# Performance work log

Hardware: AMD Instinct MI355X
Metric: run time of the kernel (lower is better)

Reference implementation:

```python
import jax, jax.numpy as jnp
import numpy as np

N_NODES = 100000
N_EDGES = 1000000
IN, HID, HEADS, OUT = 256, 32, 4, 40
HH = HID * HEADS  # 128
NEG_SLOPE = 0.2


def gat_conv(x, W, al, ar, b, src, dst, heads):
    """DGL-style GATConv. x:[N,Din] W:[Din,heads*F] al/ar/b:[heads,F]. Returns [N,heads,F]."""
    N = x.shape[0]
    h = (x @ W).reshape(N, heads, -1)                      # [N,H,F]
    el = (h * al).sum(-1)                                  # [N,H]
    er = (h * ar).sum(-1)                                  # [N,H]
    e = jax.nn.leaky_relu(el[src] + er[dst], NEG_SLOPE)    # [E,H]
    # segment softmax over incoming edges of each dst node
    m = jax.ops.segment_max(e, dst, num_segments=N)        # [N,H]
    m = jnp.where(jnp.isfinite(m), m, 0.0)                 # nodes w/o in-edges
    ex = jnp.exp(e - m[dst])                               # [E,H]
    s = jax.ops.segment_sum(ex, dst, num_segments=N)       # [N,H]
    alpha = ex / jnp.where(s[dst] == 0, 1.0, s[dst])       # [E,H]
    out = jax.ops.segment_sum(alpha[:, :, None] * h[src], dst, num_segments=N)
    return out + b                                          # [N,H,F]


def setup_inputs() -> dict:
    key = jax.random.key(0)
    ks = jax.random.split(key, 12)
    p = lambda k, shape, fan: jax.random.normal(k, shape, jnp.float32) / np.float32(np.sqrt(fan))
    features = jax.random.normal(ks[0], (N_NODES, IN), jnp.float32)
    src = jax.random.randint(ks[1], (N_EDGES,), 0, N_NODES, jnp.int32)
    dst = jax.random.randint(ks[2], (N_EDGES,), 0, N_NODES, jnp.int32)
    W1 = p(ks[3], (IN, HH), IN)
    al1 = p(ks[4], (HEADS, HID), HID)
    ar1 = p(ks[5], (HEADS, HID), HID)
    b1 = jnp.zeros((HEADS, HID), jnp.float32)
    W2 = p(ks[6], (HH, HH), HH)
    al2 = p(ks[7], (HEADS, HID), HID)
    ar2 = p(ks[8], (HEADS, HID), HID)
    b2 = jnp.zeros((HEADS, HID), jnp.float32)
    W3 = p(ks[9], (HH, OUT), HH)
    al3 = p(ks[10], (1, OUT), OUT)
    ar3 = p(ks[11], (1, OUT), OUT)
    b3 = jnp.zeros((1, OUT), jnp.float32)
    return dict(features=features, W1=W1, al1=al1, ar1=ar1, b1=b1,
                W2=W2, al2=al2, ar2=ar2, b2=b2,
                W3=W3, al3=al3, ar3=ar3, b3=b3, src=src, dst=dst)


def reference(features, W1, al1, ar1, b1, W2, al2, ar2, b2, W3, al3, ar3, b3, src, dst):
    N = features.shape[0]
    h = jax.nn.relu(gat_conv(features, W1, al1, ar1, b1, src, dst, HEADS).reshape(N, -1))
    h = jax.nn.relu(gat_conv(h, W2, al2, ar2, b2, src, dst, HEADS).reshape(N, -1))
    # dropout: eval mode -> identity
    h = gat_conv(h, W3, al3, ar3, b3, src, dst, 1).mean(1)  # [N,OUT]
    return jax.nn.log_softmax(h, axis=1)
```

## Files before the change

kernel.cpp:

```cpp
#include <hip/hip_runtime.h>
#include <hip/hip_bf16.h>
#include <math.h>

#define NN 100000
#define NE 1000000
#define CAP 128
#define NPB 512
#define NBUC ((NN + NPB - 1) / NPB)
#define CAPB 8192
#define P1B 512
#define P1E ((NE + P1B - 1) / P1B)

typedef __attribute__((ext_vector_type(8))) short bf16x8;
typedef __attribute__((ext_vector_type(4))) float f32x4;
typedef unsigned int u32;
typedef unsigned short u16;
typedef unsigned long long u64;

__device__ __forceinline__ u16 f2b(float f) {
    __hip_bfloat16 h = __float2bfloat16(f);
    return *reinterpret_cast<u16*>(&h);
}
__device__ __forceinline__ float b2f(u16 u) {
    __hip_bfloat16 h = *reinterpret_cast<__hip_bfloat16*>(&u);
    return __bfloat162float(h);
}
__device__ __forceinline__ float bflo(u32 v) { return __uint_as_float(v << 16); }
__device__ __forceinline__ float bfhi(u32 v) { return __uint_as_float(v & 0xffff0000u); }


__global__ void hist_kernel(const int* __restrict__ dst, int* __restrict__ deg, int E) {
    int i = blockIdx.x * blockDim.x + threadIdx.x;
    if (i < E) atomicAdd(&deg[dst[i]], 1);
}

__global__ void scan_local(const int* __restrict__ deg, int* __restrict__ rowptr,
                           int* __restrict__ bsum, int N) {
    __shared__ int s[256];
    int i = blockIdx.x * 256 + threadIdx.x;
    int v = (i < N) ? deg[i] : 0;
    s[threadIdx.x] = v;
    __syncthreads();
    #pragma unroll
    for (int off = 1; off < 256; off <<= 1) {
        int t = (threadIdx.x >= off) ? s[threadIdx.x - off] : 0;
        __syncthreads();
        s[threadIdx.x] += t;
        __syncthreads();
    }
    if (i < N) rowptr[i + 1] = s[threadIdx.x];
    if (threadIdx.x == 255) bsum[blockIdx.x] = s[255];
}

__global__ void scan_bsum(int* __restrict__ bsum, int NB) {
    __shared__ int s[512];
    int v = (threadIdx.x < NB) ? bsum[threadIdx.x] : 0;
    s[threadIdx.x] = v;
    __syncthreads();
    for (int off = 1; off < 512; off <<= 1) {
        int t = (threadIdx.x >= off) ? s[threadIdx.x - off] : 0;
        __syncthreads();
        s[threadIdx.x] += t;
        __syncthreads();
    }
    if (threadIdx.x < NB) bsum[threadIdx.x] = s[threadIdx.x] - v;
}

__global__ void scan_add(int* __restrict__ rowptr, const int* __restrict__ bsum, int N) {
    int i = blockIdx.x * blockDim.x + threadIdx.x;
    if (i < N) rowptr[i + 1] += bsum[i >> 8];
    if (i == 0) rowptr[0] = 0;
}


__global__ void initcur(const int* __restrict__ rowptr, int* __restrict__ gcur) {
    int b = threadIdx.x;
    if (b < NBUC) gcur[b] = rowptr[b << 9];
}

__global__ __launch_bounds__(256) void part1(const int* __restrict__ src,
                                             const int* __restrict__ dst,
                                             int* __restrict__ gcur,
                                             long long* __restrict__ ebuf) {
    __shared__ int cnt[256], sex[256], base[256], cur2[256], scn[256];
    __shared__ long long stage[P1E];
    const int tid = threadIdx.x;
    const int e0 = blockIdx.x * P1E;
    const int e1 = min(e0 + P1E, NE);
    cnt[tid] = 0;
    __syncthreads();
    for (int i = e0 + tid; i < e1; i += 256)
        atomicAdd(&cnt[dst[i] >> 9], 1);
    __syncthreads();
    int v = cnt[tid];
    scn[tid] = v;
    __syncthreads();
    #pragma unroll
    for (int off = 1; off < 256; off <<= 1) {
        int t = (tid >= off) ? scn[tid - off] : 0;
        __syncthreads();
        scn[tid] += t;
        __syncthreads();
    }
    sex[tid] = scn[tid] - v;
    if (tid < NBUC) base[tid] = (v > 0) ? atomicAdd(&gcur[tid], v) : 0;
    cur2[tid] = 0;
    __syncthreads();
    for (int i = e0 + tid; i < e1; i += 256) {
        int d = dst[i], s = src[i];
        int b = d >> 9;
        int slot = sex[b] + atomicAdd(&cur2[b], 1);
        stage[slot] = ((long long)(u32)d << 32) | (u32)s;
    }
    __syncthreads();
    const int tot = e1 - e0;
    for (int i = tid; i < tot; i += 256) {
        long long ll = stage[i];
        int b = (int)((u64)ll >> 32) >> 9;
        ebuf[(size_t)base[b] + (i - sex[b])] = ll;
    }
}

__global__ __launch_bounds__(256) void part2(const int* __restrict__ rowptr,
                                             const long long* __restrict__ ebuf,
                                             int* __restrict__ csrc) {
    __shared__ int nb[NPB], cnt[NPB];
    __shared__ int stage[CAPB];
    const int tid = threadIdx.x;
    const int n0 = blockIdx.x << 9;
    const int nn = min(NPB, NN - n0);
    const int estart = rowptr[n0];
    const int eend = rowptr[n0 + nn];
    const int tot = eend - estart;
    for (int i = tid; i < nn; i += 256) {
        nb[i] = rowptr[n0 + i] - estart;
        cnt[i] = 0;
    }
    __syncthreads();
    if (tot <= CAPB) {
        for (int i = estart + tid; i < eend; i += 256) {
            long long ll = ebuf[i];
            int ln = (int)((u64)ll >> 32) - n0;
            int pos = nb[ln] + atomicAdd(&cnt[ln], 1);
            stage[pos] = (int)ll;
        }
        __syncthreads();
        for (int i = tid; i < tot; i += 256) csrc[estart + i] = stage[i];
    } else {
        for (int i = estart + tid; i < eend; i += 256) {
            long long ll = ebuf[i];
            int ln = (int)((u64)ll >> 32) - n0;
            int pos = nb[ln] + atomicAdd(&cnt[ln], 1);
            csrc[estart + pos] = (int)ll;
        }
    }
}


__global__ void transW3(const float* __restrict__ W1, u16* __restrict__ W1t,
                        const float* __restrict__ W2, u16* __restrict__ W2t,
                        const float* __restrict__ W3, u16* __restrict__ W3t) {
    int idx = blockIdx.x * 256 + threadIdx.x;
    if (idx < 32768) {
        int n = idx / 256, k = idx % 256;
        W1t[idx] = f2b(W1[(size_t)k * 128 + n]);
    } else if (idx < 32768 + 16384) {
        int j = idx - 32768;
        int n = j / 128, k = j % 128;
        W2t[j] = f2b(W2[(size_t)k * 128 + n]);
    } else if (idx < 32768 + 16384 + 6144) {
        int j = idx - 32768 - 16384;
        int n = j / 128, k = j % 128;
        W3t[j] = f2b((n < 40) ? W3[(size_t)k * 40 + n] : 0.f);
    }
}

template<int K, int NT, int OUTW, bool AF32, int NH>
__global__ __launch_bounds__(256, 4) void gemm_s(const void* __restrict__ Ap_,
                                                 const u16* __restrict__ Wt,
                                                 const float* __restrict__ al,
                                                 const float* __restrict__ ar,
                                                 u16* __restrict__ C,
                                                 float* __restrict__ el,
                                                 float* __restrict__ er, int M) {
    constexpr int KC = 128;
    constexpr int NKC = K / KC;
    constexpr int NB = NT * 16;
    constexpr int CHK = KC / 8;
    __shared__ u16 lB[NB * KC];
    const int tid = threadIdx.x;
    const int w = tid >> 6, l = tid & 63;
    const int lr = l & 15, lq = l >> 4;
    const int row0 = blockIdx.x * 64 + w * 16;
    const u16* Ab = (const u16*)Ap_;
    const float* Af = (const float*)Ap_;

    int gr0 = row0 + lr; if (gr0 >= M) gr0 = M - 1;
    const size_t aoff = (size_t)gr0 * K;

    f32x4 acc[NT] = {};
    #pragma unroll
    for (int kc = 0; kc < NKC; ++kc) {
        for (int idx = tid; idx < NB * CHK; idx += 256) {
            int row = idx / CHK, c = idx % CHK;
            float4 v = *reinterpret_cast<const float4*>(&Wt[(size_t)row * K + kc * KC + c * 8]);
            int cs = c ^ (row & 7);
            *reinterpret_cast<float4*>(&lB[row * KC + cs * 8]) = v;
        }
        __syncthreads();
        bf16x8 a0, a1, a2, a3;
        if (AF32) {
            float4 v[8];
            #pragma unroll
            for (int i = 0; i < 8; ++i)
                v[i] = *reinterpret_cast<const float4*>(
                    &Af[aoff + kc * KC + (i >> 1) * 32 + lq * 8 + (i & 1) * 4]);
            bf16x8 t[4];
            #pragma unroll
            for (int i = 0; i < 4; ++i) {
                t[i][0] = (short)f2b(v[2 * i].x); t[i][1] = (short)f2b(v[2 * i].y);
                t[i][2] = (short)f2b(v[2 * i].z); t[i][3] = (short)f2b(v[2 * i].w);
                t[i][4] = (short)f2b(v[2 * i + 1].x); t[i][5] = (short)f2b(v[2 * i + 1].y);
                t[i][6] = (short)f2b(v[2 * i + 1].z); t[i][7] = (short)f2b(v[2 * i + 1].w);
            }
            a0 = t[0]; a1 = t[1]; a2 = t[2]; a3 = t[3];
        } else {
            a0 = *reinterpret_cast<const bf16x8*>(&Ab[aoff + kc * KC + 0 * 32 + lq * 8]);
            a1 = *reinterpret_cast<const bf16x8*>(&Ab[aoff + kc * KC + 1 * 32 + lq * 8]);
            a2 = *reinterpret_cast<const bf16x8*>(&Ab[aoff + kc * KC + 2 * 32 + lq * 8]);
            a3 = *reinterpret_cast<const bf16x8*>(&Ab[aoff + kc * KC + 3 * 32 + lq * 8]);
        }
        #pragma unroll
        for (int ks = 0; ks < 4; ++ks) {
            bf16x8 aF = (ks == 0) ? a0 : (ks == 1) ? a1 : (ks == 2) ? a2 : a3;
            const int cs = (ks * 4 + lq) ^ (lr & 7);
            #pragma unroll
            for (int nr = 0; nr < NT; ++nr) {
                bf16x8 bF = *reinterpret_cast<const bf16x8*>(&lB[(nr * 16 + lr) * KC + cs * 8]);
                acc[nr] = __builtin_amdgcn_mfma_f32_16x16x32_bf16(aF, bF, acc[nr], 0, 0, 0);
            }
        }
        if (kc + 1 < NKC) __syncthreads();
    }

    float alv[NT], arv[NT];
    #pragma unroll
    for (int nr = 0; nr < NT; ++nr) {
        int c = nr * 16 + lr;
        alv[nr] = (c < OUTW) ? al[c] : 0.f;
        arv[nr] = (c < OUTW) ? ar[c] : 0.f;
    }
    #pragma unroll
    for (int reg = 0; reg < 4; ++reg) {
        int gr = row0 + lq * 4 + reg;
        bool ok = gr < M;
        if (ok) {
            #pragma unroll
            for (int nr = 0; nr < NT; ++nr) {
                int gc = nr * 16 + lr;
                if (gc < OUTW) C[(size_t)gr * OUTW + gc] = f2b(acc[nr][reg]);
            }
        }
        float pl[NH] = {}, pr[NH] = {};
        #pragma unroll
        for (int nr = 0; nr < NT; ++nr) {
            int hidx = (NH == 1) ? 0 : (nr >> 1);
            pl[hidx] = fmaf(acc[nr][reg], alv[nr], pl[hidx]);
            pr[hidx] = fmaf(acc[nr][reg], arv[nr], pr[hidx]);
        }
        #pragma unroll
        for (int o = 8; o >= 1; o >>= 1) {
            #pragma unroll
            for (int hh = 0; hh < NH; ++hh) {
                pl[hh] += __shfl_xor(pl[hh], o);
                pr[hh] += __shfl_xor(pr[hh], o);
            }
        }
        if (ok && lr == 0) {
            #pragma unroll
            for (int hh = 0; hh < NH; ++hh) {
                el[gr * NH + hh] = pl[hh];
                er[gr * NH + hh] = pr[hh];
            }
        }
    }
}


template<bool RELU>
__global__ __launch_bounds__(256) void agg4v5(const char* __restrict__ hbase,
                                              const float4* __restrict__ el4,
                                              const float4* __restrict__ er4,
                                              const float* __restrict__ bias,
                                              const int* __restrict__ rowptr,
                                              const int* __restrict__ csrc,
                                              u32* __restrict__ out, int N) {
    __shared__ u32 s_ed[4][CAP][8];
    const int wslot = threadIdx.x >> 6, lane = threadIdx.x & 63;
    const int wid = blockIdx.x * 4 + wslot;
    if (wid >= N) return;
    const int beg = rowptr[wid];
    const int deg = rowptr[wid + 1] - beg;
    const float4 er = er4[wid];
    const int hh = lane >> 4;
    const u32 lshl = (u32)(lane << 2);
    const float2 bv = reinterpret_cast<const float2*>(bias)[lane];
    float accA, accB, invs;

    if (deg <= CAP) {
        for (int basej = 0; basej < deg; basej += 64) {
            int j = basej + lane;
            if (j < deg) {
                int sid = csrc[beg + j];
                float4 ev = el4[sid];
                float e0 = ev.x + er.x; e0 = e0 > 0.f ? e0 : 0.2f * e0;
                float e1 = ev.y + er.y; e1 = e1 > 0.f ? e1 : 0.2f * e1;
                float e2 = ev.z + er.z; e2 = e2 > 0.f ? e2 : 0.2f * e2;
                float e3 = ev.w + er.w; e3 = e3 > 0.f ? e3 : 0.2f * e3;
                u32 so = (u32)sid << 8;
                int2 v0 = make_int2(__float_as_int(__expf(e0)), (int)so);
                int2 v1 = make_int2(__float_as_int(__expf(e1)), (int)so);
                int2 v2 = make_int2(__float_as_int(__expf(e2)), (int)so);
                int2 v3 = make_int2(__float_as_int(__expf(e3)), (int)so);
                *reinterpret_cast<int2*>(&s_ed[wslot][j][0]) = v0;
                *reinterpret_cast<int2*>(&s_ed[wslot][j][2]) = v1;
                *reinterpret_cast<int2*>(&s_ed[wslot][j][4]) = v2;
                *reinterpret_cast<int2*>(&s_ed[wslot][j][6]) = v3;
            }
        }
        const u32* ebase = &s_ed[wslot][0][hh * 2];
        float a[8] = {}, b[8] = {}, sw[8] = {};
        int p = 0;
        const int deg8 = deg & ~7;
        for (; p < deg8; p += 8) {
            #pragma unroll
            for (int k = 0; k < 8; ++k) {
                int2 rv = *reinterpret_cast<const int2*>(ebase + (p + k) * 8);
                float wg = __int_as_float(rv.x);
                u32 hv = *reinterpret_cast<const u32*>(hbase + ((u32)rv.y | lshl));
                a[k] = fmaf(wg, bflo(hv), a[k]);
                b[k] = fmaf(wg, bfhi(hv), b[k]);
                sw[k] += wg;
            }
        }
        for (; p < deg; ++p) {
            int2 rv = *reinterpret_cast<const int2*>(ebase + p * 8);
            float wg = __int_as_float(rv.x);
            u32 hv = *reinterpret_cast<const u32*>(hbase + ((u32)rv.y | lshl));
            a[0] = fmaf(wg, bflo(hv), a[0]);
            b[0] = fmaf(wg, bfhi(hv), b[0]);
            sw[0] += wg;
        }
        accA = ((a[0] + a[1]) + (a[2] + a[3])) + ((a[4] + a[5]) + (a[6] + a[7]));
        accB = ((b[0] + b[1]) + (b[2] + b[3])) + ((b[4] + b[5]) + (b[6] + b[7]));
        float s = ((sw[0] + sw[1]) + (sw[2] + sw[3])) + ((sw[4] + sw[5]) + (sw[6] + sw[7]));
        invs = (deg > 0) ? 1.f / s : 0.f;
    } else {
        float er_h = hh == 0 ? er.x : hh == 1 ? er.y : hh == 2 ? er.z : er.w;
        float s = 0.f;
        accA = 0.f; accB = 0.f;
        for (int q = beg; q < beg + deg; ++q) {
            int sid = csrc[q];
            float4 ev = el4[sid];
            float e = (hh == 0 ? ev.x : hh == 1 ? ev.y : hh == 2 ? ev.z : ev.w) + er_h;
            e = e > 0.f ? e : 0.2f * e;
            float pe = __expf(e);
            u32 hv = *reinterpret_cast<const u32*>(hbase + (((u32)sid << 8) | lshl));
            s += pe;
            accA = fmaf(pe, bflo(hv), accA);
            accB = fmaf(pe, bfhi(hv), accB);
        }
        invs = 1.f / s;
    }
    float oA = accA * invs + bv.x;
    float oB = accB * invs + bv.y;
    if (RELU) { oA = fmaxf(oA, 0.f); oB = fmaxf(oB, 0.f); }
    out[(size_t)wid * 64 + lane] = ((u32)f2b(oB) << 16) | (u32)f2b(oA);
}

__global__ __launch_bounds__(256) void agg1v5(const char* __restrict__ hbase,
                                              const float* __restrict__ el,
                                              const float* __restrict__ er,
                                              const float* __restrict__ bias,
                                              const int* __restrict__ rowptr,
                                              const int* __restrict__ csrc,
                                              float* __restrict__ out, int N) {
    __shared__ u32 s_ed[4][CAP][2];
    const int wslot = threadIdx.x >> 6, lane = threadIdx.x & 63;
    const int wid = blockIdx.x * 4 + wslot;
    if (wid >= N) return;
    const int beg = rowptr[wid];
    const int deg = rowptr[wid + 1] - beg;
    const float ern = er[wid];
    const int ll = lane < 40 ? lane : 39;
    const u32 lloff = (u32)(ll << 1);
    float acc, invs;

    if (deg <= CAP) {
        for (int basej = 0; basej < deg; basej += 64) {
            int j = basej + lane;
            if (j < deg) {
                int sid = csrc[beg + j];
                float e = el[sid] + ern; e = e > 0.f ? e : 0.2f * e;
                u32 so = (u32)sid * 80u;
                *reinterpret_cast<int2*>(&s_ed[wslot][j][0]) =
                    make_int2(__float_as_int(__expf(e)), (int)so);
            }
        }
        const u32* ebase = &s_ed[wslot][0][0];
        float a[8] = {}, sw[8] = {};
        int p = 0;
        const int deg8 = deg & ~7;
        for (; p < deg8; p += 8) {
            #pragma unroll
            for (int k = 0; k < 8; ++k) {
                int2 rv = *reinterpret_cast<const int2*>(ebase + (p + k) * 2);
                float wg = __int_as_float(rv.x);
                u16 hv = *reinterpret_cast<const u16*>(hbase + ((u32)rv.y + lloff));
                a[k] = fmaf(wg, b2f(hv), a[k]);
                sw[k] += wg;
            }
        }
        for (; p < deg; ++p) {
            int2 rv = *reinterpret_cast<const int2*>(ebase + p * 2);
            float wg = __int_as_float(rv.x);
            u16 hv = *reinterpret_cast<const u16*>(hbase + ((u32)rv.y + lloff));
            a[0] = fmaf(wg, b2f(hv), a[0]);
            sw[0] += wg;
        }
        acc = ((a[0] + a[1]) + (a[2] + a[3])) + ((a[4] + a[5]) + (a[6] + a[7]));
        float s = ((sw[0] + sw[1]) + (sw[2] + sw[3])) + ((sw[4] + sw[5]) + (sw[6] + sw[7]));
        invs = (deg > 0) ? 1.f / s : 0.f;
    } else {
        float s = 0.f;
        acc = 0.f;
        for (int q = beg; q < beg + deg; ++q) {
            int sid = csrc[q];
            float e = el[sid] + ern; e = e > 0.f ? e : 0.2f * e;
            float pe = __expf(e);
            u16 hv = *reinterpret_cast<const u16*>(hbase + ((u32)sid * 80u + lloff));
            s += pe;
            acc = fmaf(pe, b2f(hv), acc);
        }
        invs = 1.f / s;
    }
    float v = acc * invs + ((lane < 40) ? bias[lane] : 0.f);
    float vv = (lane < 40) ? v : -INFINITY;
    float mx = vv;
    #pragma unroll
    for (int o = 32; o >= 1; o >>= 1) mx = fmaxf(mx, __shfl_xor(mx, o));
    float ex = (lane < 40) ? __expf(v - mx) : 0.f;
    float se = ex;
    #pragma unroll
    for (int o = 32; o >= 1; o >>= 1) se += __shfl_xor(se, o);
    if (lane < 40) out[(size_t)wid * 40 + lane] = v - mx - logf(se);
}


extern "C" void kernel_launch(void* const* d_in, const int* in_sizes, int n_in,
                              void* d_out, int out_size, void* d_ws, size_t ws_size,
                              hipStream_t stream) {
    const float* feat = (const float*)d_in[0];
    const float* W1  = (const float*)d_in[1];
    const float* al1 = (const float*)d_in[2];
    const float* ar1 = (const float*)d_in[3];
    const float* b1  = (const float*)d_in[4];
    const float* W2  = (const float*)d_in[5];
    const float* al2 = (const float*)d_in[6];
    const float* ar2 = (const float*)d_in[7];
    const float* b2  = (const float*)d_in[8];
    const float* W3  = (const float*)d_in[9];
    const float* al3 = (const float*)d_in[10];
    const float* ar3 = (const float*)d_in[11];
    const float* b3  = (const float*)d_in[12];
    const int*   src = (const int*)d_in[13];
    const int*   dst = (const int*)d_in[14];
    float* out = (float*)d_out;
    const int N = NN, E = NE;

    char* ws = (char*)d_ws;
    size_t off = 0;
    auto alloc = [&](size_t bytes) -> char* {
        char* p = ws + off;
        off += (bytes + 255) & ~(size_t)255;
        return p;
    };
    int* deg    = (int*)alloc((size_t)N * 4);
    int* rowptr = (int*)alloc((size_t)(N + 1) * 4);
    int* bsum   = (int*)alloc(512 * 4);
    int* gcur   = (int*)alloc(256 * 4);
    int* csrc   = (int*)alloc((size_t)E * 4);
    long long* ebuf = (long long*)alloc((size_t)E * 8);
    float* el   = (float*)alloc((size_t)N * 4 * 4);
    float* er   = (float*)alloc((size_t)N * 4 * 4);
    u16* hb     = (u16*)alloc((size_t)N * 128 * 2);
    u16* xb     = (u16*)alloc((size_t)N * 128 * 2);
    u16* h3     = (u16*)alloc((size_t)N * 40 * 2 + 256);
    u16* W1t    = (u16*)alloc((size_t)128 * 256 * 2);
    u16* W2t    = (u16*)alloc((size_t)128 * 128 * 2);
    u16* W3t    = (u16*)alloc((size_t)48 * 128 * 2);

    hipMemsetAsync(deg, 0, (size_t)N * 4, stream);
    hist_kernel<<<(E + 255) / 256, 256, 0, stream>>>(dst, deg, E);
    int NB = (N + 255) / 256;
    scan_local<<<NB, 256, 0, stream>>>(deg, rowptr, bsum, N);
    scan_bsum<<<1, 512, 0, stream>>>(bsum, NB);
    scan_add<<<(N + 255) / 256, 256, 0, stream>>>(rowptr, bsum, N);
    initcur<<<1, 256, 0, stream>>>(rowptr, gcur);
    part1<<<P1B, 256, 0, stream>>>(src, dst, gcur, ebuf);
    part2<<<NBUC, 256, 0, stream>>>(rowptr, ebuf, csrc);

    transW3<<<(32768 + 16384 + 6144 + 255) / 256, 256, 0, stream>>>(W1, W1t, W2, W2t, W3, W3t);

    int gemmGrid = (N + 63) / 64;
    int nodeGrid = (N + 3) / 4;

    gemm_s<256, 8, 128, true, 4><<<gemmGrid, 256, 0, stream>>>(feat, W1t, al1, ar1, hb, el, er, N);
    agg4v5<true><<<nodeGrid, 256, 0, stream>>>((const char*)hb, (const float4*)el, (const float4*)er,
                                               b1, rowptr, csrc, (u32*)xb, N);

    gemm_s<128, 8, 128, false, 4><<<gemmGrid, 256, 0, stream>>>(xb, W2t, al2, ar2, hb, el, er, N);
    agg4v5<true><<<nodeGrid, 256, 0, stream>>>((const char*)hb, (const float4*)el, (const float4*)er,
                                               b2, rowptr, csrc, (u32*)xb, N);

    gemm_s<128, 3, 40, false, 1><<<gemmGrid, 256, 0, stream>>>(xb, W3t, al3, ar3, h3, el, er, N);
    agg1v5<<<nodeGrid, 256, 0, stream>>>((const char*)h3, el, er, b3, rowptr, csrc, out, N);
}
```

Measured before the change: 330.7 us.

## Build CSR from bucket counts and aggregate two nodes per wave with block-shared edge staging

The per-node histogram and three-stage scan are replaced by a coarse 512-node bucket count and a single-block scan. Per-node row pointers are now computed inside the second partition pass with a local count and scan. The aggregation kernels handle 8 nodes per block (two per wave). Edge weights for the whole block are staged cooperatively in shared memory, and the two nodes' gathers are interleaved to increase memory-level parallelism. This cuts launch count and atomic traffic in CSR construction, at the cost of an extra ebuf read pass and more register use in the aggregation kernels.

```diff
diff --git a/kernel.cpp b/kernel.cpp
--- a/kernel.cpp
+++ b/kernel.cpp
@@ -4,12 +4,12 @@
 
 #define NN 100000
 #define NE 1000000
-#define CAP 128
 #define NPB 512
 #define NBUC ((NN + NPB - 1) / NPB)
 #define CAPB 8192
 #define P1B 512
 #define P1E ((NE + P1B - 1) / P1B)
+#define BCAP 512
 
 typedef __attribute__((ext_vector_type(8))) short bf16x8;
 typedef __attribute__((ext_vector_type(4))) float f32x4;
@@ -29,54 +29,39 @@
 __device__ __forceinline__ float bfhi(u32 v) { return __uint_as_float(v & 0xffff0000u); }
 
 
-__global__ void hist_kernel(const int* __restrict__ dst, int* __restrict__ deg, int E) {
-    int i = blockIdx.x * blockDim.x + threadIdx.x;
-    if (i < E) atomicAdd(&deg[dst[i]], 1);
-}
-
-__global__ void scan_local(const int* __restrict__ deg, int* __restrict__ rowptr,
-                           int* __restrict__ bsum, int N) {
+__global__ void bucket_cnt(const int* __restrict__ dst, int* __restrict__ bcnt, int E) {
+    __shared__ int c[NBUC];
+    for (int i = threadIdx.x; i < NBUC; i += 256) c[i] = 0;
+    __syncthreads();
+    int i = blockIdx.x * 256 + threadIdx.x;
+    const int stride = gridDim.x * 256;
+    for (; i < E; i += stride) atomicAdd(&c[dst[i] >> 9], 1);
+    __syncthreads();
+    for (int j = threadIdx.x; j < NBUC; j += 256)
+        if (c[j]) atomicAdd(&bcnt[j], c[j]);
+}
+
+__global__ void bucket_scan(const int* __restrict__ bcnt, int* __restrict__ bbase,
+                            int* __restrict__ gcur) {
     __shared__ int s[256];
-    int i = blockIdx.x * 256 + threadIdx.x;
-    int v = (i < N) ? deg[i] : 0;
-    s[threadIdx.x] = v;
-    __syncthreads();
-    #pragma unroll
+    const int tid = threadIdx.x;
+    int v = (tid < NBUC) ? bcnt[tid] : 0;
+    s[tid] = v;
+    __syncthreads();
     for (int off = 1; off < 256; off <<= 1) {
-        int t = (threadIdx.x >= off) ? s[threadIdx.x - off] : 0;
-        __syncthreads();
-        s[threadIdx.x] += t;
-        __syncthreads();
-    }
-    if (i < N) rowptr[i + 1] = s[threadIdx.x];
-    if (threadIdx.x == 255) bsum[blockIdx.x] = s[255];
-}
-
-__global__ void scan_bsum(int* __restrict__ bsum, int NB) {
-    __shared__ int s[512];
-    int v = (threadIdx.x < NB) ? bsum[threadIdx.x] : 0;
-    s[threadIdx.x] = v;
-    __syncthreads();
-    for (int off = 1; off < 512; off <<= 1) {
-        int t = (threadIdx.x >= off) ? s[threadIdx.x - off] : 0;
-        __syncthreads();
-        s[threadIdx.x] += t;
-        __syncthreads();
-    }
-    if (threadIdx.x < NB) bsum[threadIdx.x] = s[threadIdx.x] - v;
-}
-
-__global__ void scan_add(int* __restrict__ rowptr, const int* __restrict__ bsum, int N) {
-    int i = blockIdx.x * blockDim.x + threadIdx.x;
-    if (i < N) rowptr[i + 1] += bsum[i >> 8];
-    if (i == 0) rowptr[0] = 0;
-}
-
-
-__global__ void initcur(const int* __restrict__ rowptr, int* __restrict__ gcur) {
-    int b = threadIdx.x;
-    if (b < NBUC) gcur[b] = rowptr[b << 9];
-}
+        int t = (tid >= off) ? s[tid - off] : 0;
+        __syncthreads();
+        s[tid] += t;
+        __syncthreads();
+    }
+    if (tid < NBUC) {
+        int excl = s[tid] - v;
+        bbase[tid] = excl;
+        gcur[tid] = excl;
+    }
+    if (tid == NBUC - 1) bbase[NBUC] = s[tid];
+}
+
 
 __global__ __launch_bounds__(256) void part1(const int* __restrict__ src,
                                              const int* __restrict__ dst,
@@ -121,21 +106,45 @@
     }
 }
 
-__global__ __launch_bounds__(256) void part2(const int* __restrict__ rowptr,
-                                             const long long* __restrict__ ebuf,
-                                             int* __restrict__ csrc) {
+__global__ __launch_bounds__(256) void part2B(const int* __restrict__ bbase,
+                                              const long long* __restrict__ ebuf,
+                                              int* __restrict__ rowptr,
+                                              int* __restrict__ csrc) {
     __shared__ int nb[NPB], cnt[NPB];
     __shared__ int stage[CAPB];
+    __shared__ int ssum[256];
     const int tid = threadIdx.x;
     const int n0 = blockIdx.x << 9;
     const int nn = min(NPB, NN - n0);
-    const int estart = rowptr[n0];
-    const int eend = rowptr[n0 + nn];
+    const int estart = bbase[blockIdx.x];
+    const int eend = bbase[blockIdx.x + 1];
     const int tot = eend - estart;
-    for (int i = tid; i < nn; i += 256) {
-        nb[i] = rowptr[n0 + i] - estart;
-        cnt[i] = 0;
-    }
+    for (int i = tid; i < NPB; i += 256) cnt[i] = 0;
+    __syncthreads();
+    for (int i = estart + tid; i < eend; i += 256) {
+        int ln = (int)((u64)ebuf[i] >> 32) - n0;
+        atomicAdd(&cnt[ln], 1);
+    }
+    __syncthreads();
+    int a = cnt[2 * tid], b = cnt[2 * tid + 1];
+    int ts = a + b;
+    ssum[tid] = ts;
+    __syncthreads();
+    #pragma unroll
+    for (int off = 1; off < 256; off <<= 1) {
+        int t = (tid >= off) ? ssum[tid - off] : 0;
+        __syncthreads();
+        ssum[tid] += t;
+        __syncthreads();
+    }
+    int eb = ssum[tid] - ts;
+    nb[2 * tid] = eb;
+    nb[2 * tid + 1] = eb + a;
+    if (2 * tid < nn)     rowptr[n0 + 2 * tid]     = estart + eb;
+    if (2 * tid + 1 < nn) rowptr[n0 + 2 * tid + 1] = estart + eb + a;
+    if (tid == 0 && blockIdx.x == gridDim.x - 1) rowptr[NN] = eend;
+    __syncthreads();
+    for (int i = tid; i < NPB; i += 256) cnt[i] = 0;
     __syncthreads();
     if (tot <= CAPB) {
         for (int i = estart + tid; i < eend; i += 256) {
@@ -288,172 +297,256 @@
 
 
 template<bool RELU>
-__global__ __launch_bounds__(256) void agg4v5(const char* __restrict__ hbase,
+__global__ __launch_bounds__(256) void agg4v6(const char* __restrict__ hbase,
                                               const float4* __restrict__ el4,
                                               const float4* __restrict__ er4,
                                               const float* __restrict__ bias,
                                               const int* __restrict__ rowptr,
                                               const int* __restrict__ csrc,
                                               u32* __restrict__ out, int N) {
-    __shared__ u32 s_ed[4][CAP][8];
-    const int wslot = threadIdx.x >> 6, lane = threadIdx.x & 63;
-    const int wid = blockIdx.x * 4 + wslot;
-    if (wid >= N) return;
-    const int beg = rowptr[wid];
-    const int deg = rowptr[wid + 1] - beg;
-    const float4 er = er4[wid];
+    __shared__ u32 s_ed[BCAP][8];
+    __shared__ int s_off[9];
+    const int tid = threadIdx.x, w = tid >> 6, lane = tid & 63;
+    const int base = blockIdx.x * 8;
+    if (tid < 9) {
+        int n = base + tid;
+        s_off[tid] = rowptr[n <= N ? n : N];
+    }
+    __syncthreads();
+    const int beg_blk = s_off[0];
+    const int T = s_off[8] - beg_blk;
     const int hh = lane >> 4;
     const u32 lshl = (u32)(lane << 2);
     const float2 bv = reinterpret_cast<const float2*>(bias)[lane];
-    float accA, accB, invs;
-
-    if (deg <= CAP) {
-        for (int basej = 0; basej < deg; basej += 64) {
-            int j = basej + lane;
-            if (j < deg) {
-                int sid = csrc[beg + j];
+    const bool small = (T <= BCAP);
+
+    if (small) {
+        for (int t = tid; t < T; t += 256) {
+            int sid = csrc[beg_blk + t];
+            int nd = 0;
+            #pragma unroll
+            for (int k = 1; k < 8; ++k) nd += (t >= (s_off[k] - beg_blk)) ? 1 : 0;
+            float4 er = er4[base + nd];
+            float4 ev = el4[sid];
+            float e0 = ev.x + er.x; e0 = e0 > 0.f ? e0 : 0.2f * e0;
+            float e1 = ev.y + er.y; e1 = e1 > 0.f ? e1 : 0.2f * e1;
+            float e2 = ev.z + er.z; e2 = e2 > 0.f ? e2 : 0.2f * e2;
+            float e3 = ev.w + er.w; e3 = e3 > 0.f ? e3 : 0.2f * e3;
+            u32 so = (u32)sid << 8;
+            *reinterpret_cast<int2*>(&s_ed[t][0]) = make_int2(__float_as_int(__expf(e0)), (int)so);
+            *reinterpret_cast<int2*>(&s_ed[t][2]) = make_int2(__float_as_int(__expf(e1)), (int)so);
+            *reinterpret_cast<int2*>(&s_ed[t][4]) = make_int2(__float_as_int(__expf(e2)), (int)so);
+            *reinterpret_cast<int2*>(&s_ed[t][6]) = make_int2(__float_as_int(__expf(e3)), (int)so);
+        }
+    }
+    __syncthreads();
+
+    const int nA = base + 2 * w;
+    if (nA >= N) return;
+    const int nB = nA + 1;
+    float aA[4] = {}, bA[4] = {}, sA[4] = {};
+    float aB[4] = {}, bB[4] = {}, sB[4] = {};
+
+    if (small) {
+        const int oA0 = s_off[2 * w] - beg_blk, oA1 = s_off[2 * w + 1] - beg_blk;
+        const int oB0 = oA1, oB1 = s_off[2 * w + 2] - beg_blk;
+        const int dA = oA1 - oA0, dB = oB1 - oB0;
+        const int it = max((dA + 3) >> 2, (dB + 3) >> 2);
+        for (int i = 0; i < it; ++i) {
+            const int pA = oA0 + i * 4, pB = oB0 + i * 4;
+            #pragma unroll
+            for (int k = 0; k < 4; ++k) {
+                int j = pA + k; bool v = j < oA1;
+                int2 rv = *reinterpret_cast<const int2*>(&s_ed[v ? j : 0][hh * 2]);
+                float wg = v ? __int_as_float(rv.x) : 0.f;
+                u32 hv = *reinterpret_cast<const u32*>(hbase + ((u32)rv.y | lshl));
+                aA[k] = fmaf(wg, bflo(hv), aA[k]);
+                bA[k] = fmaf(wg, bfhi(hv), bA[k]);
+                sA[k] += wg;
+            }
+            #pragma unroll
+            for (int k = 0; k < 4; ++k) {
+                int j = pB + k; bool v = j < oB1;
+                int2 rv = *reinterpret_cast<const int2*>(&s_ed[v ? j : 0][hh * 2]);
+                float wg = v ? __int_as_float(rv.x) : 0.f;
+                u32 hv = *reinterpret_cast<const u32*>(hbase + ((u32)rv.y | lshl));
+                aB[k] = fmaf(wg, bflo(hv), aB[k]);
+                bB[k] = fmaf(wg, bfhi(hv), bB[k]);
+                sB[k] += wg;
+            }
+        }
+        {
+            float accA = (aA[0] + aA[1]) + (aA[2] + aA[3]);
+            float accB = (bA[0] + bA[1]) + (bA[2] + bA[3]);
+            float s = (sA[0] + sA[1]) + (sA[2] + sA[3]);
+            float invs = (dA > 0) ? 1.f / s : 0.f;
+            float oA = accA * invs + bv.x;
+            float oB = accB * invs + bv.y;
+            if (RELU) { oA = fmaxf(oA, 0.f); oB = fmaxf(oB, 0.f); }
+            out[(size_t)nA * 64 + lane] = ((u32)f2b(oB) << 16) | (u32)f2b(oA);
+        }
+        {
+            float accA = (aB[0] + aB[1]) + (aB[2] + aB[3]);
+            float accB = (bB[0] + bB[1]) + (bB[2] + bB[3]);
+            float s = (sB[0] + sB[1]) + (sB[2] + sB[3]);
+            float invs = (dB > 0) ? 1.f / s : 0.f;
+            float oA = accA * invs + bv.x;
+            float oB = accB * invs + bv.y;
+            if (RELU) { oA = fmaxf(oA, 0.f); oB = fmaxf(oB, 0.f); }
+            if (nB < N)
+                out[(size_t)nB * 64 + lane] = ((u32)f2b(oB) << 16) | (u32)f2b(oA);
+        }
+    } else {
+        #pragma unroll
+        for (int which = 0; which < 2; ++which) {
+            int nd = nA + which;
+            if (nd >= N) break;
+            int beg = s_off[2 * w + which], end = s_off[2 * w + which + 1];
+            float4 er = er4[nd];
+            float er_h = hh == 0 ? er.x : hh == 1 ? er.y : hh == 2 ? er.z : er.w;
+            float s = 0.f, accA = 0.f, accB = 0.f;
+            for (int q = beg; q < end; ++q) {
+                int sid = csrc[q];
                 float4 ev = el4[sid];
-                float e0 = ev.x + er.x; e0 = e0 > 0.f ? e0 : 0.2f * e0;
-                float e1 = ev.y + er.y; e1 = e1 > 0.f ? e1 : 0.2f * e1;
-                float e2 = ev.z + er.z; e2 = e2 > 0.f ? e2 : 0.2f * e2;
-                float e3 = ev.w + er.w; e3 = e3 > 0.f ? e3 : 0.2f * e3;
-                u32 so = (u32)sid << 8;
-                int2 v0 = make_int2(__float_as_int(__expf(e0)), (int)so);
-                int2 v1 = make_int2(__float_as_int(__expf(e1)), (int)so);
-                int2 v2 = make_int2(__float_as_int(__expf(e2)), (int)so);
-                int2 v3 = make_int2(__float_as_int(__expf(e3)), (int)so);
-                *reinterpret_cast<int2*>(&s_ed[wslot][j][0]) = v0;
-                *reinterpret_cast<int2*>(&s_ed[wslot][j][2]) = v1;
-                *reinterpret_cast<int2*>(&s_ed[wslot][j][4]) = v2;
-                *reinterpret_cast<int2*>(&s_ed[wslot][j][6]) = v3;
-            }
-        }
-        const u32* ebase = &s_ed[wslot][0][hh * 2];
-        float a[8] = {}, b[8] = {}, sw[8] = {};
-        int p = 0;
-        const int deg8 = deg & ~7;
-        for (; p < deg8; p += 8) {
-            #pragma unroll
-            for (int k = 0; k < 8; ++k) {
-                int2 rv = *reinterpret_cast<const int2*>(ebase + (p + k) * 8);
-                float wg = __int_as_float(rv.x);
-                u32 hv = *reinterpret_cast<const u32*>(hbase + ((u32)rv.y | lshl));
-                a[k] = fmaf(wg, bflo(hv), a[k]);
-                b[k] = fmaf(wg, bfhi(hv), b[k]);
-                sw[k] += wg;
-            }
-        }
-        for (; p < deg; ++p) {
-            int2 rv = *reinterpret_cast<const int2*>(ebase + p * 8);
-            float wg = __int_as_float(rv.x);
-            u32 hv = *reinterpret_cast<const u32*>(hbase + ((u32)rv.y | lshl));
-            a[0] = fmaf(wg, bflo(hv), a[0]);
-            b[0] = fmaf(wg, bfhi(hv), b[0]);
-            sw[0] += wg;
-        }
-        accA = ((a[0] + a[1]) + (a[2] + a[3])) + ((a[4] + a[5]) + (a[6] + a[7]));
-        accB = ((b[0] + b[1]) + (b[2] + b[3])) + ((b[4] + b[5]) + (b[6] + b[7]));
-        float s = ((sw[0] + sw[1]) + (sw[2] + sw[3])) + ((sw[4] + sw[5]) + (sw[6] + sw[7]));
-        invs = (deg > 0) ? 1.f / s : 0.f;
-    } else {
-        float er_h = hh == 0 ? er.x : hh == 1 ? er.y : hh == 2 ? er.z : er.w;
-        float s = 0.f;
-        accA = 0.f; accB = 0.f;
-        for (int q = beg; q < beg + deg; ++q) {
-            int sid = csrc[q];
-            float4 ev = el4[sid];
-            float e = (hh == 0 ? ev.x : hh == 1 ? ev.y : hh == 2 ? ev.z : ev.w) + er_h;
-            e = e > 0.f ? e : 0.2f * e;
-            float pe = __expf(e);
-            u32 hv = *reinterpret_cast<const u32*>(hbase + (((u32)sid << 8) | lshl));
-            s += pe;
-            accA = fmaf(pe, bflo(hv), accA);
-            accB = fmaf(pe, bfhi(hv), accB);
-        }
-        invs = 1.f / s;
-    }
-    float oA = accA * invs + bv.x;
-    float oB = accB * invs + bv.y;
-    if (RELU) { oA = fmaxf(oA, 0.f); oB = fmaxf(oB, 0.f); }
-    out[(size_t)wid * 64 + lane] = ((u32)f2b(oB) << 16) | (u32)f2b(oA);
-}
-
-__global__ __launch_bounds__(256) void agg1v5(const char* __restrict__ hbase,
+                float e = (hh == 0 ? ev.x : hh == 1 ? ev.y : hh == 2 ? ev.z : ev.w) + er_h;
+                e = e > 0.f ? e : 0.2f * e;
+                float pe = __expf(e);
+                u32 hv = *reinterpret_cast<const u32*>(hbase + (((u32)sid << 8) | lshl));
+                s += pe;
+                accA = fmaf(pe, bflo(hv), accA);
+                accB = fmaf(pe, bfhi(hv), accB);
+            }
+            float invs = (end > beg) ? 1.f / s : 0.f;
+            float oA = accA * invs + bv.x;
+            float oB = accB * invs + bv.y;
+            if (RELU) { oA = fmaxf(oA, 0.f); oB = fmaxf(oB, 0.f); }
+            out[(size_t)nd * 64 + lane] = ((u32)f2b(oB) << 16) | (u32)f2b(oA);
+        }
+    }
+}
+
+__global__ __launch_bounds__(256) void agg1v6(const char* __restrict__ hbase,
                                               const float* __restrict__ el,
                                               const float* __restrict__ er,
                                               const float* __restrict__ bias,
                                               const int* __restrict__ rowptr,
                                               const int* __restrict__ csrc,
                                               float* __restrict__ out, int N) {
-    __shared__ u32 s_ed[4][CAP][2];
-    const int wslot = threadIdx.x >> 6, lane = threadIdx.x & 63;
-    const int wid = blockIdx.x * 4 + wslot;
-    if (wid >= N) return;
-    const int beg = rowptr[wid];
-    const int deg = rowptr[wid + 1] - beg;
-    const float ern = er[wid];
+    __shared__ u32 s_e1[BCAP][2];
+    __shared__ int s_off[9];
+    const int tid = threadIdx.x, w = tid >> 6, lane = tid & 63;
+    const int base = blockIdx.x * 8;
+    if (tid < 9) {
+        int n = base + tid;
+        s_off[tid] = rowptr[n <= N ? n : N];
+    }
+    __syncthreads();
+    const int beg_blk = s_off[0];
+    const int T = s_off[8] - beg_blk;
     const int ll = lane < 40 ? lane : 39;
     const u32 lloff = (u32)(ll << 1);
-    float acc, invs;
-
-    if (deg <= CAP) {
-        for (int basej = 0; basej < deg; basej += 64) {
-            int j = basej + lane;
-            if (j < deg) {
-                int sid = csrc[beg + j];
+    const float bvv = (lane < 40) ? bias[lane] : 0.f;
+    const bool small = (T <= BCAP);
+
+    if (small) {
+        for (int t = tid; t < T; t += 256) {
+            int sid = csrc[beg_blk + t];
+            int nd = 0;
+            #pragma unroll
+            for (int k = 1; k < 8; ++k) nd += (t >= (s_off[k] - beg_blk)) ? 1 : 0;
+            float e = el[sid] + er[base + nd];
+            e = e > 0.f ? e : 0.2f * e;
+            *reinterpret_cast<int2*>(&s_e1[t][0]) =
+                make_int2(__float_as_int(__expf(e)), (int)((u32)sid * 80u));
+        }
+    }
+    __syncthreads();
+
+    const int nA = base + 2 * w;
+    if (nA >= N) return;
+    const int nB = nA + 1;
+    float aA[4] = {}, sA[4] = {}, aB[4] = {}, sB[4] = {};
+    float accA, invsA, accB, invsB;
+    bool haveB = (nB < N);
+
+    if (small) {
+        const int oA0 = s_off[2 * w] - beg_blk, oA1 = s_off[2 * w + 1] - beg_blk;
+        const int oB0 = oA1, oB1 = s_off[2 * w + 2] - beg_blk;
+        const int dA = oA1 - oA0, dB = oB1 - oB0;
+        const int it = max((dA + 3) >> 2, (dB + 3) >> 2);
+        for (int i = 0; i < it; ++i) {
+            const int pA = oA0 + i * 4, pB = oB0 + i * 4;
+            #pragma unroll
+            for (int k = 0; k < 4; ++k) {
+                int j = pA + k; bool v = j < oA1;
+                int2 rv = *reinterpret_cast<const int2*>(&s_e1[v ? j : 0][0]);
+                float wg = v ? __int_as_float(rv.x) : 0.f;
+                u16 hv = *reinterpret_cast<const u16*>(hbase + ((u32)rv.y + lloff));
+                aA[k] = fmaf(wg, b2f(hv), aA[k]);
+                sA[k] += wg;
+            }
+            #pragma unroll
+            for (int k = 0; k < 4; ++k) {
+                int j = pB + k; bool v = j < oB1;
+                int2 rv = *reinterpret_cast<const int2*>(&s_e1[v ? j : 0][0]);
+                float wg = v ? __int_as_float(rv.x) : 0.f;
+                u16 hv = *reinterpret_cast<const u16*>(hbase + ((u32)rv.y + lloff));
+                aB[k] = fmaf(wg, b2f(hv), aB[k]);
+                sB[k] += wg;
+            }
+        }
+        accA = (aA[0] + aA[1]) + (aA[2] + aA[3]);
+        float ssA = (sA[0] + sA[1]) + (sA[2] + sA[3]);
+        invsA = (dA > 0) ? 1.f / ssA : 0.f;
+        accB = (aB[0] + aB[1]) + (aB[2] + aB[3]);
+        float ssB = (sB[0] + sB[1]) + (sB[2] + sB[3]);
+        invsB = (dB > 0) ? 1.f / ssB : 0.f;
+    } else {
+        accA = 0.f; accB = 0.f; invsA = 0.f; invsB = 0.f;
+        #pragma unroll
+        for (int which = 0; which < 2; ++which) {
+            int nd = nA + which;
+            if (nd >= N) break;
+            int beg = s_off[2 * w + which], end = s_off[2 * w + which + 1];
+            float ern = er[nd];
+            float s = 0.f, acc = 0.f;
+            for (int q = beg; q < end; ++q) {
+                int sid = csrc[q];
                 float e = el[sid] + ern; e = e > 0.f ? e : 0.2f * e;
-                u32 so = (u32)sid * 80u;
-                *reinterpret_cast<int2*>(&s_ed[wslot][j][0]) =
-                    make_int2(__float_as_int(__expf(e)), (int)so);
-            }
-        }
-        const u32* ebase = &s_ed[wslot][0][0];
-        float a[8] = {}, sw[8] = {};
-        int p = 0;
-        const int deg8 = deg & ~7;
-        for (; p < deg8; p += 8) {
-            #pragma unroll
-            for (int k = 0; k < 8; ++k) {
-                int2 rv = *reinterpret_cast<const int2*>(ebase + (p + k) * 2);
-                float wg = __int_as_float(rv.x);
-                u16 hv = *reinterpret_cast<const u16*>(hbase + ((u32)rv.y + lloff));
-                a[k] = fmaf(wg, b2f(hv), a[k]);
-                sw[k] += wg;
-            }
-        }
-        for (; p < deg; ++p) {
-            int2 rv = *reinterpret_cast<const int2*>(ebase + p * 2);
-            float wg = __int_as_float(rv.x);
-            u16 hv = *reinterpret_cast<const u16*>(hbase + ((u32)rv.y + lloff));
-            a[0] = fmaf(wg, b2f(hv), a[0]);
-            sw[0] += wg;
-        }
-        acc = ((a[0] + a[1]) + (a[2] + a[3])) + ((a[4] + a[5]) + (a[6] + a[7]));
-        float s = ((sw[0] + sw[1]) + (sw[2] + sw[3])) + ((sw[4] + sw[5]) + (sw[6] + sw[7]));
-        invs = (deg > 0) ? 1.f / s : 0.f;
-    } else {
-        float s = 0.f;
-        acc = 0.f;
-        for (int q = beg; q < beg + deg; ++q) {
-            int sid = csrc[q];
-            float e = el[sid] + ern; e = e > 0.f ? e : 0.2f * e;
-            float pe = __expf(e);
-            u16 hv = *reinterpret_cast<const u16*>(hbase + ((u32)sid * 80u + lloff));
-            s += pe;
-            acc = fmaf(pe, b2f(hv), acc);
-        }
-        invs = 1.f / s;
-    }
-    float v = acc * invs + ((lane < 40) ? bias[lane] : 0.f);
-    float vv = (lane < 40) ? v : -INFINITY;
-    float mx = vv;
-    #pragma unroll
-    for (int o = 32; o >= 1; o >>= 1) mx = fmaxf(mx, __shfl_xor(mx, o));
-    float ex = (lane < 40) ? __expf(v - mx) : 0.f;
-    float se = ex;
-    #pragma unroll
-    for (int o = 32; o >= 1; o >>= 1) se += __shfl_xor(se, o);
-    if (lane < 40) out[(size_t)wid * 40 + lane] = v - mx - logf(se);
+                float pe = __expf(e);
+                u16 hv = *reinterpret_cast<const u16*>(hbase + ((u32)sid * 80u + lloff));
+                s += pe;
+                acc = fmaf(pe, b2f(hv), acc);
+            }
+            float inv = (end > beg) ? 1.f / s : 0.f;
+            if (which == 0) { accA = acc; invsA = inv; }
+            else { accB = acc; invsB = inv; }
+        }
+    }
+    {
+        float v = accA * invsA + bvv;
+        float vv = (lane < 40) ? v : -INFINITY;
+        float mx = vv;
+        #pragma unroll
+        for (int o = 32; o >= 1; o >>= 1) mx = fmaxf(mx, __shfl_xor(mx, o));
+        float ex = (lane < 40) ? __expf(v - mx) : 0.f;
+        float se = ex;
+        #pragma unroll
+        for (int o = 32; o >= 1; o >>= 1) se += __shfl_xor(se, o);
+        if (lane < 40) out[(size_t)nA * 40 + lane] = v - mx - logf(se);
+    }
+    if (haveB) {
+        float v = accB * invsB + bvv;
+        float vv = (lane < 40) ? v : -INFINITY;
+        float mx = vv;
+        #pragma unroll
+        for (int o = 32; o >= 1; o >>= 1) mx = fmaxf(mx, __shfl_xor(mx, o));
+        float ex = (lane < 40) ? __expf(v - mx) : 0.f;
+        float se = ex;
+        #pragma unroll
+        for (int o = 32; o >= 1; o >>= 1) se += __shfl_xor(se, o);
+        if (lane < 40) out[(size_t)nB * 40 + lane] = v - mx - logf(se);
+    }
 }
 
 
@@ -485,10 +578,10 @@
         off += (bytes + 255) & ~(size_t)255;
         return p;
     };
-    int* deg    = (int*)alloc((size_t)N * 4);
+    int* bcnt   = (int*)alloc(256 * 4);
+    int* bbase  = (int*)alloc(256 * 4);
+    int* gcur   = (int*)alloc(256 * 4);
     int* rowptr = (int*)alloc((size_t)(N + 1) * 4);
-    int* bsum   = (int*)alloc(512 * 4);
-    int* gcur   = (int*)alloc(256 * 4);
     int* csrc   = (int*)alloc((size_t)E * 4);
     long long* ebuf = (long long*)alloc((size_t)E * 8);
     float* el   = (float*)alloc((size_t)N * 4 * 4);
@@ -500,29 +593,25 @@
     u16* W2t    = (u16*)alloc((size_t)128 * 128 * 2);
     u16* W3t    = (u16*)alloc((size_t)48 * 128 * 2);
 
-    hipMemsetAsync(deg, 0, (size_t)N * 4, stream);
-    hist_kernel<<<(E + 255) / 256, 256, 0, stream>>>(dst, deg, E);
-    int NB = (N + 255) / 256;
-    scan_local<<<NB, 256, 0, stream>>>(deg, rowptr, bsum, N);
-    scan_bsum<<<1, 512, 0, stream>>>(bsum, NB);
-    scan_add<<<(N + 255) / 256, 256, 0, stream>>>(rowptr, bsum, N);
-    initcur<<<1, 256, 0, stream>>>(rowptr, gcur);
+    hipMemsetAsync(bcnt, 0, NBUC * 4, stream);
+    bucket_cnt<<<1024, 256, 0, stream>>>(dst, bcnt, E);
+    bucket_scan<<<1, 256, 0, stream>>>(bcnt, bbase, gcur);
     part1<<<P1B, 256, 0, stream>>>(src, dst, gcur, ebuf);
-    part2<<<NBUC, 256, 0, stream>>>(rowptr, ebuf, csrc);
+    part2B<<<NBUC, 256, 0, stream>>>(bbase, ebuf, rowptr, csrc);
 
     transW3<<<(32768 + 16384 + 6144 + 255) / 256, 256, 0, stream>>>(W1, W1t, W2, W2t, W3, W3t);
 
     int gemmGrid = (N + 63) / 64;
-    int nodeGrid = (N + 3) / 4;
+    int aggGrid = (N + 7) / 8;
 
     gemm_s<256, 8, 128, true, 4><<<gemmGrid, 256, 0, stream>>>(feat, W1t, al1, ar1, hb, el, er, N);
-    agg4v5<true><<<nodeGrid, 256, 0, stream>>>((const char*)hb, (const float4*)el, (const float4*)er,
-                                               b1, rowptr, csrc, (u32*)xb, N);
+    agg4v6<true><<<aggGrid, 256, 0, stream>>>((const char*)hb, (const float4*)el, (const float4*)er,
+                                              b1, rowptr, csrc, (u32*)xb, N);
 
     gemm_s<128, 8, 128, false, 4><<<gemmGrid, 256, 0, stream>>>(xb, W2t, al2, ar2, hb, el, er, N);
-    agg4v5<true><<<nodeGrid, 256, 0, stream>>>((const char*)hb, (const float4*)el, (const float4*)er,
-                                               b2, rowptr, csrc, (u32*)xb, N);
+    agg4v6<true><<<aggGrid, 256, 0, stream>>>((const char*)hb, (const float4*)el, (const float4*)er,
+                                              b2, rowptr, csrc, (u32*)xb, N);
 
     gemm_s<128, 3, 40, false, 1><<<gemmGrid, 256, 0, stream>>>(xb, W3t, al3, ar3, h3, el, er, N);
-    agg1v5<<<nodeGrid, 256, 0, stream>>>((const char*)h3, el, er, b3, rowptr, csrc, out, N);
-}
+    agg1v6<<<aggGrid, 256, 0, stream>>>((const char*)h3, el, er, b3, rowptr, csrc, out, N);
+}
```

After: 268.7 us. -18.8%, faster.
